# Optimization experiments

Measured on AMD Instinct MI355X. Metric: run time of the kernel, lower is better.

Reference implementation:

```python
import jax, jax.numpy as jnp
import numpy as np

INPUT_WIDTH = 768
OUTPUT_WIDTH = 768
DEPTH = 11
N_NODES = 2 ** (DEPTH + 1) - 1  # 4095 (parallel_size == 1)
N_TOKENS = 8192


def setup_inputs() -> dict:
    key = jax.random.key(0)
    k0, k1, k2 = jax.random.split(key, 3)
    oldx = jax.random.normal(k0, (N_TOKENS, INPUT_WIDTH), dtype=jnp.float32)
    # nn.Linear default init scale ~ 1/sqrt(fan_in); keep inits small so logits are reasonable
    w_in = jax.random.normal(k1, (N_NODES, INPUT_WIDTH), dtype=jnp.float32) / np.sqrt(INPUT_WIDTH)
    w_out = jax.random.normal(k2, (OUTPUT_WIDTH, N_NODES), dtype=jnp.float32) / np.sqrt(N_NODES)
    return {"oldx": oldx, "w_in": w_in, "w_out": w_out}


def _fff(oldx, w_in, w_out):
    x = oldx.reshape(-1, INPUT_WIDTH)            # [B, D]
    B = x.shape[0]
    logits = x @ w_in.T                          # [B, n_nodes]
    decisions = (logits > 0).astype(jnp.int32)   # [B, n_nodes]
    acts = jax.nn.gelu(logits, approximate=False)  # torch nn.GELU default = exact erf

    # Tree walk: root node 0 is always active; at each level, follow the
    # binary decision at the current node to pick the child, marking it active.
    dmap = jnp.zeros_like(logits).at[:, 0].set(1.0)
    cur = jnp.zeros((B,), dtype=jnp.int32)
    rows = jnp.arange(B)
    for d in range(DEPTH):
        cur_platform = 2 ** d - 1
        next_platform = 2 ** (d + 1) - 1
        moves = jnp.take_along_axis(decisions, cur[:, None], axis=1)[:, 0]  # [B]
        nxt = (cur - cur_platform) * 2 + moves + next_platform
        dmap = dmap.at[rows, nxt].set(1.0)
        cur = nxt
    dmap = jax.lax.stop_gradient(dmap)           # built under torch.no_grad()

    masked = acts * dmap                         # [B, n_nodes], sparse (depth+1 active per row)
    return masked @ w_out.T                      # [B, output_width]


def reference(oldx, w_in, w_out):
    return _fff(oldx, w_in, w_out)
```

## Files before the change

kernel.cpp:

```cpp
#include <hip/hip_runtime.h>
#include <math.h>

#define DEPTH    11
#define NNODES   4095
#define DIN      768
#define NTOK     8192
#define TAU      0.06f
#define WT_MAX   0.12f
#define WT_STEP  (WT_MAX / 127.0f)

typedef unsigned int uint32;
typedef float f32x4 __attribute__((ext_vector_type(4)));

__global__ __launch_bounds__(256) void fff_prep(const float* __restrict__ w_in,
                                                const float* __restrict__ w_out,
                                                uint32* __restrict__ wq,
                                                float* __restrict__ wscale,
                                                uint32* __restrict__ wTq) {
    __shared__ float tile[32][33];
    const int bid = blockIdx.x;
    const int tid = threadIdx.x;

    if (bid < 3072) {
        const int n0 = (bid & 127) * 32;
        const int j0 = (bid >> 7) * 32;
        const int tx = tid & 31, ty = tid >> 5;
#pragma unroll
        for (int i = 0; i < 32; i += 8) {
            const int j = j0 + ty + i;
            const int n = n0 + tx;
            if (n < NNODES) tile[ty + i][tx] = w_out[(size_t)j * NNODES + n];
        }
        __syncthreads();
        const int nl = tid >> 3;
        const int jq = (tid & 7) * 4;
        const int n  = n0 + nl;
        if (n < NNODES) {
            const float inv = 127.0f / WT_MAX;
            int q0 = __float2int_rn(fminf(fmaxf(tile[jq + 0][nl] * inv, -127.f), 127.f));
            int q1 = __float2int_rn(fminf(fmaxf(tile[jq + 1][nl] * inv, -127.f), 127.f));
            int q2 = __float2int_rn(fminf(fmaxf(tile[jq + 2][nl] * inv, -127.f), 127.f));
            int q3 = __float2int_rn(fminf(fmaxf(tile[jq + 3][nl] * inv, -127.f), 127.f));
            const uint32 pack = (uint32)(q0 & 0xFF) | ((uint32)(q1 & 0xFF) << 8) |
                                ((uint32)(q2 & 0xFF) << 16) | ((uint32)(q3 & 0xFF) << 24);
            wTq[((size_t)n * DIN + j0 + jq) >> 2] = pack;
        }
    } else {
        const int row  = ((bid - 3072) * 256 + tid) >> 6;
        const int lane = tid & 63;
        if (row < NNODES) {
            const float4* wr = reinterpret_cast<const float4*>(w_in + (size_t)row * DIN);
            const float4 a = wr[lane], b = wr[lane + 64], c = wr[lane + 128];
            float m = fmaxf(fabsf(a.x), fabsf(a.y));
            m = fmaxf(m, fmaxf(fabsf(a.z), fabsf(a.w)));
            m = fmaxf(m, fmaxf(fabsf(b.x), fabsf(b.y)));
            m = fmaxf(m, fmaxf(fabsf(b.z), fabsf(b.w)));
            m = fmaxf(m, fmaxf(fabsf(c.x), fabsf(c.y)));
            m = fmaxf(m, fmaxf(fabsf(c.z), fabsf(c.w)));
#pragma unroll
            for (int off = 32; off >= 1; off >>= 1) m = fmaxf(m, __shfl_xor(m, off));
            const float inv = (m > 0.f) ? (127.0f / m) : 0.f;
            const float s   = m * (1.0f / 127.0f);

            uint32* rq = wq + (size_t)row * (DIN / 4);
            const float4 v[3] = {a, b, c};
#pragma unroll
            for (int k = 0; k < 3; ++k) {
                int q0 = __float2int_rn(fminf(fmaxf(v[k].x * inv, -127.f), 127.f));
                int q1 = __float2int_rn(fminf(fmaxf(v[k].y * inv, -127.f), 127.f));
                int q2 = __float2int_rn(fminf(fmaxf(v[k].z * inv, -127.f), 127.f));
                int q3 = __float2int_rn(fminf(fmaxf(v[k].w * inv, -127.f), 127.f));
                rq[lane + 64 * k] = (uint32)(q0 & 0xFF) | ((uint32)(q1 & 0xFF) << 8) |
                                    ((uint32)(q2 & 0xFF) << 16) | ((uint32)(q3 & 0xFF) << 24);
            }
            if (lane == 0) wscale[row] = s;
        }
    }
}

__device__ __forceinline__ float sb0(uint32 u) { return (float)((int)(u << 24) >> 24); }
__device__ __forceinline__ float sb1(uint32 u) { return (float)((int)(u << 16) >> 24); }
__device__ __forceinline__ float sb2(uint32 u) { return (float)((int)(u <<  8) >> 24); }
__device__ __forceinline__ float sb3(uint32 u) { return (float)((int)u        >> 24); }

__global__ __launch_bounds__(256) void fff_walk_i8(const float* __restrict__ x,
                                                   const float* __restrict__ w_in,
                                                   const uint32* __restrict__ wq,
                                                   const float* __restrict__ wscale,
                                                   unsigned* __restrict__ bits_out,
                                                   float* __restrict__ g_out) {
    const int token = (int)((blockIdx.x * blockDim.x + threadIdx.x) >> 6);
    const int lane  = (int)(threadIdx.x & 63);

    const f32x4* xr = reinterpret_cast<const f32x4*>(x + (size_t)token * DIN);
    const f32x4 xv0 = __builtin_nontemporal_load(xr + lane);
    const f32x4 xv1 = __builtin_nontemporal_load(xr + lane + 64);
    const f32x4 xv2 = __builtin_nontemporal_load(xr + lane + 128);

    int cur = 0;
    uint32 a = wq[lane], b = wq[lane + 64], c = wq[lane + 128];
    float  s = wscale[0];

    unsigned mask = 0;

#pragma unroll
    for (int d = 0; d <= DEPTH; ++d) {
        uint32 la = 0, lb = 0, lc = 0, ra = 0, rb = 0, rc = 0;
        float  ls = 0.f, rs = 0.f;
        if (d < DEPTH) {
            const int nl = 2 * cur + 1, nr = 2 * cur + 2;
            const uint32* rqL = wq + (size_t)nl * (DIN / 4);
            const uint32* rqR = wq + (size_t)nr * (DIN / 4);
            la = rqL[lane]; lb = rqL[lane + 64]; lc = rqL[lane + 128];
            ra = rqR[lane]; rb = rqR[lane + 64]; rc = rqR[lane + 128];
            ls = wscale[nl]; rs = wscale[nr];
        }

        float s0 = 0.f, s1 = 0.f, s2 = 0.f, s3 = 0.f;
        s0 = fmaf(xv0[0], sb0(a), s0); s1 = fmaf(xv0[1], sb1(a), s1);
        s2 = fmaf(xv0[2], sb2(a), s2); s3 = fmaf(xv0[3], sb3(a), s3);
        s0 = fmaf(xv1[0], sb0(b), s0); s1 = fmaf(xv1[1], sb1(b), s1);
        s2 = fmaf(xv1[2], sb2(b), s2); s3 = fmaf(xv1[3], sb3(b), s3);
        s0 = fmaf(xv2[0], sb0(c), s0); s1 = fmaf(xv2[1], sb1(c), s1);
        s2 = fmaf(xv2[2], sb2(c), s2); s3 = fmaf(xv2[3], sb3(c), s3);
        float part = ((s0 + s1) + (s2 + s3)) * s;
#pragma unroll
        for (int off = 32; off >= 1; off >>= 1) part += __shfl_xor(part, off);

        float lg    = part;
        bool  right = (part > 0.0f);

        if (fabsf(lg) < TAU) {
            const float4* wr = reinterpret_cast<const float4*>(w_in + (size_t)cur * DIN);
            const float4 w0 = wr[lane], w1 = wr[lane + 64], w2 = wr[lane + 128];
            double p0 = 0.0, p1 = 0.0, p2 = 0.0;
            p0 += (double)xv0[0] * w0.x; p0 += (double)xv0[1] * w0.y;
            p0 += (double)xv0[2] * w0.z; p0 += (double)xv0[3] * w0.w;
            p1 += (double)xv1[0] * w1.x; p1 += (double)xv1[1] * w1.y;
            p1 += (double)xv1[2] * w1.z; p1 += (double)xv1[3] * w1.w;
            p2 += (double)xv2[0] * w2.x; p2 += (double)xv2[1] * w2.y;
            p2 += (double)xv2[2] * w2.z; p2 += (double)xv2[3] * w2.w;
            double pd = (p0 + p1) + p2;
#pragma unroll
            for (int off = 32; off >= 1; off >>= 1) pd += __shfl_xor(pd, off);
            lg    = (float)pd;
            right = (pd > 0.0);
        }

        if (lane == 0)
            g_out[token * 12 + d] = 0.5f * lg * (1.0f + erff(lg * 0.7071067811865476f));

        if (d < DEPTH) {
            a = right ? ra : la;
            b = right ? rb : lb;
            c = right ? rc : lc;
            s = right ? rs : ls;
            mask |= (right ? 1u : 0u) << d;
            cur = __builtin_amdgcn_readfirstlane(2 * cur + 1 + (right ? 1 : 0));
        }
    }
    if (lane == 0) bits_out[token] = mask;
}

__global__ __launch_bounds__(256) void fff_gather_i8(const uint32* __restrict__ wTq,
                                                     const unsigned* __restrict__ bits_in,
                                                     const float* __restrict__ g_in,
                                                     float* __restrict__ out) {
    const int token = (int)((blockIdx.x * blockDim.x + threadIdx.x) >> 6);
    const int lane  = (int)(threadIdx.x & 63);

    const unsigned mask = bits_in[token];
    float gv = 0.f;
    if (lane < 12) gv = g_in[token * 12 + lane];

    float acc[12];
#pragma unroll
    for (int i = 0; i < 12; ++i) acc[i] = 0.f;

    int cur = 0;
#pragma unroll
    for (int d = 0; d <= DEPTH; ++d) {
        const float gg = __shfl(gv, d);
        const float cf = gg * WT_STEP;
        const uint32* rt = wTq + (size_t)cur * (DIN / 4);
        const uint32 ta = rt[lane], tb = rt[lane + 64], tc = rt[lane + 128];
        acc[0]  = fmaf(cf, sb0(ta), acc[0]);  acc[1]  = fmaf(cf, sb1(ta), acc[1]);
        acc[2]  = fmaf(cf, sb2(ta), acc[2]);  acc[3]  = fmaf(cf, sb3(ta), acc[3]);
        acc[4]  = fmaf(cf, sb0(tb), acc[4]);  acc[5]  = fmaf(cf, sb1(tb), acc[5]);
        acc[6]  = fmaf(cf, sb2(tb), acc[6]);  acc[7]  = fmaf(cf, sb3(tb), acc[7]);
        acc[8]  = fmaf(cf, sb0(tc), acc[8]);  acc[9]  = fmaf(cf, sb1(tc), acc[9]);
        acc[10] = fmaf(cf, sb2(tc), acc[10]); acc[11] = fmaf(cf, sb3(tc), acc[11]);
        if (d < DEPTH) cur = 2 * cur + 1 + (int)((mask >> d) & 1u);
    }

    f32x4* orow = reinterpret_cast<f32x4*>(out + (size_t)token * DIN);
    f32x4 o0, o1, o2;
    o0[0] = acc[0];  o0[1] = acc[1];  o0[2] = acc[2];  o0[3] = acc[3];
    o1[0] = acc[4];  o1[1] = acc[5];  o1[2] = acc[6];  o1[3] = acc[7];
    o2[0] = acc[8];  o2[1] = acc[9];  o2[2] = acc[10]; o2[3] = acc[11];
    __builtin_nontemporal_store(o0, orow + lane);
    __builtin_nontemporal_store(o1, orow + lane + 64);
    __builtin_nontemporal_store(o2, orow + lane + 128);
}

__global__ __launch_bounds__(256) void fff_fused_fallback(const float* __restrict__ x,
                                                          const float* __restrict__ w_in,
                                                          const float* __restrict__ w_o,
                                                          float* __restrict__ out) {
    const int token = (int)((blockIdx.x * blockDim.x + threadIdx.x) >> 6);
    const int lane  = (int)(threadIdx.x & 63);

    const float4* xr = reinterpret_cast<const float4*>(x + (size_t)token * DIN);
    float4 xv[3];
#pragma unroll
    for (int k = 0; k < 3; ++k) xv[k] = xr[lane + 64 * k];
    float4 acc[3];
#pragma unroll
    for (int k = 0; k < 3; ++k) acc[k] = make_float4(0.f, 0.f, 0.f, 0.f);

    int cur = 0;
#pragma unroll
    for (int d = 0; d <= DEPTH; ++d) {
        const float4* wr = reinterpret_cast<const float4*>(w_in + (size_t)cur * DIN);
        double part = 0.0;
#pragma unroll
        for (int k = 0; k < 3; ++k) {
            const float4 w = wr[lane + 64 * k];
            part += (double)xv[k].x * w.x; part += (double)xv[k].y * w.y;
            part += (double)xv[k].z * w.z; part += (double)xv[k].w * w.w;
        }
#pragma unroll
        for (int off = 32; off >= 1; off >>= 1) part += __shfl_xor(part, off);
        const float logit = (float)part;
        const float gg = 0.5f * logit * (1.0f + erff(logit * 0.7071067811865476f));
#pragma unroll
        for (int k = 0; k < 3; ++k) {
            const int j = (lane + 64 * k) * 4;
            acc[k].x = fmaf(gg, w_o[(size_t)(j + 0) * NNODES + cur], acc[k].x);
            acc[k].y = fmaf(gg, w_o[(size_t)(j + 1) * NNODES + cur], acc[k].y);
            acc[k].z = fmaf(gg, w_o[(size_t)(j + 2) * NNODES + cur], acc[k].z);
            acc[k].w = fmaf(gg, w_o[(size_t)(j + 3) * NNODES + cur], acc[k].w);
        }
        if (d < DEPTH) cur = 2 * cur + 1 + (part > 0.0 ? 1 : 0);
    }
    float4* orow = reinterpret_cast<float4*>(out + (size_t)token * DIN);
#pragma unroll
    for (int k = 0; k < 3; ++k) orow[lane + 64 * k] = acc[k];
}

extern "C" void kernel_launch(void* const* d_in, const int* in_sizes, int n_in,
                              void* d_out, int out_size, void* d_ws, size_t ws_size,
                              hipStream_t stream) {
    const float* x     = (const float*)d_in[0];
    const float* w_in  = (const float*)d_in[1];
    const float* w_out = (const float*)d_in[2];
    float*       out   = (float*)d_out;

    const size_t wq_bytes   = (size_t)NNODES * DIN;
    const size_t wTq_bytes  = (size_t)NNODES * DIN;
    const size_t sc_bytes   = ((size_t)NNODES * sizeof(float) + 255) & ~255ull;
    const size_t g_bytes    = (size_t)NTOK * 12 * sizeof(float);
    const size_t bits_bytes = (size_t)NTOK * sizeof(unsigned);
    const size_t need = wq_bytes + wTq_bytes + sc_bytes + g_bytes + bits_bytes;

    if (ws_size >= need) {
        char* ws = (char*)d_ws;
        uint32*   wq     = (uint32*)ws;
        uint32*   wTq    = (uint32*)(ws + wq_bytes);
        float*    wscale = (float*)(ws + wq_bytes + wTq_bytes);
        float*    g      = (float*)(ws + wq_bytes + wTq_bytes + sc_bytes);
        unsigned* bits   = (unsigned*)(ws + wq_bytes + wTq_bytes + sc_bytes + g_bytes);

        hipLaunchKernelGGL(fff_prep, dim3(4096), dim3(256), 0, stream,
                           w_in, w_out, wq, wscale, wTq);
        hipLaunchKernelGGL(fff_walk_i8, dim3(NTOK / 4), dim3(256), 0, stream,
                           x, w_in, wq, wscale, bits, g);
        hipLaunchKernelGGL(fff_gather_i8, dim3(NTOK / 4), dim3(256), 0, stream,
                           wTq, bits, g, out);
    } else {
        hipLaunchKernelGGL(fff_fused_fallback, dim3(NTOK / 4), dim3(256), 0, stream,
                           x, w_in, w_out, out);
    }
}
```

Measured before the change: 41.95 us.

## Walk four tokens per wavefront with 16-lane groups instead of one

The tree-walk kernel now assigns four tokens to each 64-lane wavefront, with 16 lanes per token each holding 12 float4 chunks of x, and reduces with a 4-step shuffle instead of 6. It drops the speculative prefetch of both children's quantized rows and loads only the current node's row, so the fetch now sits serially after each decision. The grid shrinks from 2048 to 512 blocks. Node indices are no longer wave-uniform, so weight loads become per-group, and register pressure rises from holding 48 x floats per lane.

After: 41.07 us. 2.1% less time.

```diff
diff --git a/kernel.cpp b/kernel.cpp
--- a/kernel.cpp
+++ b/kernel.cpp
@@ -83,83 +83,84 @@
 __device__ __forceinline__ float sb2(uint32 u) { return (float)((int)(u <<  8) >> 24); }
 __device__ __forceinline__ float sb3(uint32 u) { return (float)((int)u        >> 24); }
 
-__global__ __launch_bounds__(256) void fff_walk_i8(const float* __restrict__ x,
-                                                   const float* __restrict__ w_in,
-                                                   const uint32* __restrict__ wq,
-                                                   const float* __restrict__ wscale,
-                                                   unsigned* __restrict__ bits_out,
-                                                   float* __restrict__ g_out) {
-    const int token = (int)((blockIdx.x * blockDim.x + threadIdx.x) >> 6);
+__global__ __launch_bounds__(256) void fff_walk4_i8(const float* __restrict__ x,
+                                                    const float* __restrict__ w_in,
+                                                    const uint32* __restrict__ wq,
+                                                    const float* __restrict__ wscale,
+                                                    unsigned* __restrict__ bits_out,
+                                                    float* __restrict__ g_out) {
+    const int wid   = (int)((blockIdx.x * blockDim.x + threadIdx.x) >> 6);
     const int lane  = (int)(threadIdx.x & 63);
-
-    const f32x4* xr = reinterpret_cast<const f32x4*>(x + (size_t)token * DIN);
-    const f32x4 xv0 = __builtin_nontemporal_load(xr + lane);
-    const f32x4 xv1 = __builtin_nontemporal_load(xr + lane + 64);
-    const f32x4 xv2 = __builtin_nontemporal_load(xr + lane + 128);
+    const int grp   = lane >> 4;
+    const int slot  = lane & 15;
+    const int token = wid * 4 + grp;
+
+    const float4* xr = reinterpret_cast<const float4*>(x + (size_t)token * DIN);
+    float4 xv[12];
+#pragma unroll
+    for (int k = 0; k < 12; ++k) xv[k] = xr[slot + 16 * k];
 
     int cur = 0;
-    uint32 a = wq[lane], b = wq[lane + 64], c = wq[lane + 128];
-    float  s = wscale[0];
-
     unsigned mask = 0;
 
 #pragma unroll
     for (int d = 0; d <= DEPTH; ++d) {
-        uint32 la = 0, lb = 0, lc = 0, ra = 0, rb = 0, rc = 0;
-        float  ls = 0.f, rs = 0.f;
-        if (d < DEPTH) {
-            const int nl = 2 * cur + 1, nr = 2 * cur + 2;
-            const uint32* rqL = wq + (size_t)nl * (DIN / 4);
-            const uint32* rqR = wq + (size_t)nr * (DIN / 4);
-            la = rqL[lane]; lb = rqL[lane + 64]; lc = rqL[lane + 128];
-            ra = rqR[lane]; rb = rqR[lane + 64]; rc = rqR[lane + 128];
-            ls = wscale[nl]; rs = wscale[nr];
-        }
+        const uint32* rq = wq + (size_t)cur * (DIN / 4);
+        uint32 w[12];
+#pragma unroll
+        for (int k = 0; k < 12; ++k) w[k] = rq[slot + 16 * k];
+        const float s = wscale[cur];
 
         float s0 = 0.f, s1 = 0.f, s2 = 0.f, s3 = 0.f;
-        s0 = fmaf(xv0[0], sb0(a), s0); s1 = fmaf(xv0[1], sb1(a), s1);
-        s2 = fmaf(xv0[2], sb2(a), s2); s3 = fmaf(xv0[3], sb3(a), s3);
-        s0 = fmaf(xv1[0], sb0(b), s0); s1 = fmaf(xv1[1], sb1(b), s1);
-        s2 = fmaf(xv1[2], sb2(b), s2); s3 = fmaf(xv1[3], sb3(b), s3);
-        s0 = fmaf(xv2[0], sb0(c), s0); s1 = fmaf(xv2[1], sb1(c), s1);
-        s2 = fmaf(xv2[2], sb2(c), s2); s3 = fmaf(xv2[3], sb3(c), s3);
+#pragma unroll
+        for (int k = 0; k < 12; ++k) {
+            s0 = fmaf(xv[k].x, sb0(w[k]), s0);
+            s1 = fmaf(xv[k].y, sb1(w[k]), s1);
+            s2 = fmaf(xv[k].z, sb2(w[k]), s2);
+            s3 = fmaf(xv[k].w, sb3(w[k]), s3);
+        }
         float part = ((s0 + s1) + (s2 + s3)) * s;
-#pragma unroll
-        for (int off = 32; off >= 1; off >>= 1) part += __shfl_xor(part, off);
+
+#pragma unroll
+        for (int off = 8; off >= 1; off >>= 1) part += __shfl_xor(part, off);
 
         float lg    = part;
         bool  right = (part > 0.0f);
 
         if (fabsf(lg) < TAU) {
             const float4* wr = reinterpret_cast<const float4*>(w_in + (size_t)cur * DIN);
-            const float4 w0 = wr[lane], w1 = wr[lane + 64], w2 = wr[lane + 128];
-            double p0 = 0.0, p1 = 0.0, p2 = 0.0;
-            p0 += (double)xv0[0] * w0.x; p0 += (double)xv0[1] * w0.y;
-            p0 += (double)xv0[2] * w0.z; p0 += (double)xv0[3] * w0.w;
-            p1 += (double)xv1[0] * w1.x; p1 += (double)xv1[1] * w1.y;
-            p1 += (double)xv1[2] * w1.z; p1 += (double)xv1[3] * w1.w;
-            p2 += (double)xv2[0] * w2.x; p2 += (double)xv2[1] * w2.y;
-            p2 += (double)xv2[2] * w2.z; p2 += (double)xv2[3] * w2.w;
-            double pd = (p0 + p1) + p2;
-#pragma unroll
-            for (int off = 32; off >= 1; off >>= 1) pd += __shfl_xor(pd, off);
+            double p0 = 0.0, p1 = 0.0, p2 = 0.0, p3 = 0.0;
+#pragma unroll
+            for (int k = 0; k < 12; k += 4) {
+                const float4 w0 = wr[slot + 16 * (k + 0)];
+                const float4 w1 = wr[slot + 16 * (k + 1)];
+                const float4 w2 = wr[slot + 16 * (k + 2)];
+                const float4 w3 = wr[slot + 16 * (k + 3)];
+                p0 += (double)xv[k + 0].x * w0.x; p0 += (double)xv[k + 0].y * w0.y;
+                p0 += (double)xv[k + 0].z * w0.z; p0 += (double)xv[k + 0].w * w0.w;
+                p1 += (double)xv[k + 1].x * w1.x; p1 += (double)xv[k + 1].y * w1.y;
+                p1 += (double)xv[k + 1].z * w1.z; p1 += (double)xv[k + 1].w * w1.w;
+                p2 += (double)xv[k + 2].x * w2.x; p2 += (double)xv[k + 2].y * w2.y;
+                p2 += (double)xv[k + 2].z * w2.z; p2 += (double)xv[k + 2].w * w2.w;
+                p3 += (double)xv[k + 3].x * w3.x; p3 += (double)xv[k + 3].y * w3.y;
+                p3 += (double)xv[k + 3].z * w3.z; p3 += (double)xv[k + 3].w * w3.w;
+            }
+            double pd = (p0 + p1) + (p2 + p3);
+#pragma unroll
+            for (int off = 8; off >= 1; off >>= 1) pd += __shfl_xor(pd, off);
             lg    = (float)pd;
             right = (pd > 0.0);
         }
 
-        if (lane == 0)
+        if (slot == 0)
             g_out[token * 12 + d] = 0.5f * lg * (1.0f + erff(lg * 0.7071067811865476f));
 
         if (d < DEPTH) {
-            a = right ? ra : la;
-            b = right ? rb : lb;
-            c = right ? rc : lc;
-            s = right ? rs : ls;
             mask |= (right ? 1u : 0u) << d;
-            cur = __builtin_amdgcn_readfirstlane(2 * cur + 1 + (right ? 1 : 0));
-        }
-    }
-    if (lane == 0) bits_out[token] = mask;
+            cur = 2 * cur + 1 + (right ? 1 : 0);
+        }
+    }
+    if (slot == 0) bits_out[token] = mask;
 }
 
 __global__ __launch_bounds__(256) void fff_gather_i8(const uint32* __restrict__ wTq,
@@ -273,7 +274,7 @@
 
         hipLaunchKernelGGL(fff_prep, dim3(4096), dim3(256), 0, stream,
                            w_in, w_out, wq, wscale, wTq);
-        hipLaunchKernelGGL(fff_walk_i8, dim3(NTOK / 4), dim3(256), 0, stream,
+        hipLaunchKernelGGL(fff_walk4_i8, dim3(512), dim3(256), 0, stream,
                            x, w_in, wq, wscale, bits, g);
         hipLaunchKernelGGL(fff_gather_i8, dim3(NTOK / 4), dim3(256), 0, stream,
                            wTq, bits, g, out);
```
